# Kernel optimization log

Hardware: AMD Instinct MI355X
Metric: run time of the kernel (lower is better)

Reference implementation:

```python
import jax, jax.numpy as jnp
import numpy as np

D_MODEL = 1024
NUM_HEADS = 16
HEAD_DIM = D_MODEL // NUM_HEADS  # 64
THETA = 10000.0
B, S = 2, 2048


def setup_inputs() -> dict:
    key = jax.random.key(0)
    k1, k2, k3 = jax.random.split(key, 3)
    sigma_qkv = (2.0 / (D_MODEL + 3 * D_MODEL)) ** 0.5
    sigma_o = (2.0 / (D_MODEL + D_MODEL)) ** 0.5
    x = jax.random.normal(k1, (B, S, D_MODEL), dtype=jnp.float32)
    w_qkv = jax.random.normal(k2, (3 * D_MODEL, D_MODEL), dtype=jnp.float32) * sigma_qkv
    w_o = jax.random.normal(k3, (D_MODEL, D_MODEL), dtype=jnp.float32) * sigma_o
    token_positions = jnp.arange(S, dtype=jnp.int32)
    return {"x": x, "w_qkv": w_qkv, "w_o": w_o, "token_positions": token_positions, "mask": 1}


def _rope(t, pos):
    # t: (B, H, S, HEAD_DIM); pos: (S,) int
    ids = jnp.arange(HEAD_DIM // 2, dtype=jnp.float32)
    freqs = pos.astype(jnp.float32)[:, None] * (THETA ** (-2.0 * ids / HEAD_DIM))  # (S, HEAD_DIM/2)
    cos, sin = jnp.cos(freqs), jnp.sin(freqs)
    even, odd = t[..., 0::2], t[..., 1::2]
    r_even = even * cos - odd * sin
    r_odd = odd * cos + even * sin
    # interleave back to original layout
    return jnp.stack([r_even, r_odd], axis=-1).reshape(t.shape)


def reference(x, w_qkv, w_o, token_positions, mask):
    # fused QKV projection: Linear computes x @ W^T with W [out, in]
    qkv = x @ w_qkv.T  # (B, S, 3*D_MODEL)
    q, k, v = jnp.split(qkv, 3, axis=-1)

    def to_heads(t):
        return t.reshape(B, S, NUM_HEADS, HEAD_DIM).transpose(0, 2, 1, 3)  # (B, H, S, Dh)

    q, k, v = to_heads(q), to_heads(k), to_heads(v)
    q = _rope(q, token_positions)
    k = _rope(k, token_positions)

    scores = jnp.einsum('bhqd,bhkd->bhqk', q, k)
    if mask:  # causal: lower-triangular allowed
        causal = jnp.tril(jnp.ones((S, S), dtype=bool))
        scores = jnp.where(causal, scores, -jnp.inf)
    attn = jax.nn.softmax(scores * (HEAD_DIM ** -0.5), axis=-1)
    out = jnp.einsum('bhqk,bhkd->bhqd', attn, v)  # (B, H, S, Dh)
    out = out.transpose(0, 2, 1, 3).reshape(B, S, D_MODEL)
    return out @ w_o.T
```

## Files before the change

### kernel.cpp

```cpp
#include <hip/hip_runtime.h>
#include <hip/hip_bf16.h>
#include <math.h>

typedef __bf16 bf16_t;
typedef __bf16 bf16x8 __attribute__((ext_vector_type(8)));
typedef __bf16 bf16x4 __attribute__((ext_vector_type(4)));
typedef float  f32x4  __attribute__((ext_vector_type(4)));

#define D_MODEL 1024
#define NH      16
#define HD      64
#define BATCH   2
#define SEQ     2048
#define MROWS   (BATCH*SEQ)
#define QKVN    (3*D_MODEL)
#define FA_PAD  72
#define SCALE_LOG2E 0.18033688011112042f

__device__ __forceinline__ void async_cp16(const bf16_t* g, bf16_t* l) {
    __builtin_amdgcn_global_load_lds(
        (const __attribute__((address_space(1))) void*)g,
        (__attribute__((address_space(3))) void*)l,
        16, 0, 0);
}

__global__ void cvt_all(const float* __restrict__ x, const float* __restrict__ wq,
                        const float* __restrict__ wo,
                        bf16_t* __restrict__ xb, bf16_t* __restrict__ wqb,
                        bf16_t* __restrict__ wob) {
    const int nx = MROWS * D_MODEL, nq = QKVN * D_MODEL;
    int i = (blockIdx.x * blockDim.x + threadIdx.x) * 4;
    const float* s; bf16_t* d; int off;
    if (i < nx)           { s = x;  d = xb;  off = i; }
    else if (i < nx + nq) { s = wq; d = wqb; off = i - nx; }
    else                  { s = wo; d = wob; off = i - nx - nq; }
    float4 v = *(const float4*)(s + off);
    d[off]     = (bf16_t)v.x;
    d[off + 1] = (bf16_t)v.y;
    d[off + 2] = (bf16_t)v.z;
    d[off + 3] = (bf16_t)v.w;
}

template <typename OutT, int NI>
__global__ __launch_bounds__(256) void gemm_nt(const bf16_t* __restrict__ A,
                                               const bf16_t* __restrict__ Bm,
                                               OutT* __restrict__ C,
                                               int M, int N, int K) {
    __shared__ __align__(16) bf16_t As[128 * 32];
    __shared__ __align__(16) bf16_t Bs[NI * 32 * 32];
    const int tid  = threadIdx.x;
    const int w    = tid >> 6;
    const int lane = tid & 63;
    const int quad = lane >> 4;
    const int l16  = lane & 15;
    const int m0   = blockIdx.x * 128;
    const int n0   = blockIdx.y * (NI * 32);
    const int wm   = (w >> 1) * 64;
    const int wn   = (w & 1) * (NI * 16);

    f32x4 acc[4][NI];
    #pragma unroll
    for (int i = 0; i < 4; i++)
        #pragma unroll
        for (int j = 0; j < NI; j++)
            acc[i][j] = (f32x4){0.f, 0.f, 0.f, 0.f};

    const bf16_t* Ag0 = A  + (size_t)(m0 + (tid >> 2)) * K + (tid & 3) * 8;
    const bf16_t* Ag1 = Ag0 + (size_t)64 * K;
    const bf16_t* Bg0 = Bm + (size_t)(n0 + (tid >> 2)) * K + (tid & 3) * 8;
    const bf16_t* Bg1 = Bg0 + (size_t)64 * K;
    bf16_t* Al0 = &As[(size_t)tid * 8];
    bf16_t* Al1 = &As[((size_t)tid + 256) * 8];
    bf16_t* Bl0 = &Bs[(size_t)tid * 8];
    bf16_t* Bl1 = &Bs[((size_t)tid + 256) * 8];

    for (int k0 = 0; k0 < K; k0 += 32) {
        async_cp16(Ag0 + k0, Al0);
        async_cp16(Ag1 + k0, Al1);
        async_cp16(Bg0 + k0, Bl0);
        if (NI == 4) async_cp16(Bg1 + k0, Bl1);
        __syncthreads();

        bf16x8 af[4], bfr[NI];
        #pragma unroll
        for (int mi = 0; mi < 4; mi++)
            af[mi] = *(const bf16x8*)&As[(wm + mi * 16 + l16) * 32 + quad * 8];
        #pragma unroll
        for (int ni = 0; ni < NI; ni++)
            bfr[ni] = *(const bf16x8*)&Bs[(wn + ni * 16 + l16) * 32 + quad * 8];
        #pragma unroll
        for (int mi = 0; mi < 4; mi++)
            #pragma unroll
            for (int ni = 0; ni < NI; ni++)
                acc[mi][ni] = __builtin_amdgcn_mfma_f32_16x16x32_bf16(
                    af[mi], bfr[ni], acc[mi][ni], 0, 0, 0);
        __syncthreads();
    }

    #pragma unroll
    for (int mi = 0; mi < 4; mi++)
        #pragma unroll
        for (int ni = 0; ni < NI; ni++) {
            const int col = n0 + wn + ni * 16 + l16;
            #pragma unroll
            for (int r = 0; r < 4; r++) {
                const int row = m0 + wm + mi * 16 + quad * 4 + r;
                C[(size_t)row * N + col] = (OutT)acc[mi][ni][r];
            }
        }
}

__global__ __launch_bounds__(256) void rope_split(const bf16_t* __restrict__ qkv,
                                                  const int* __restrict__ pos,
                                                  bf16_t* __restrict__ Qh,
                                                  bf16_t* __restrict__ Kh,
                                                  bf16_t* __restrict__ VT) {
    __shared__ bf16_t vs[128][FA_PAD];
    const int tid   = threadIdx.x;
    const int s_loc = tid >> 1;
    const int half  = tid & 1;
    const int s0    = blockIdx.x * 128;
    const int bh    = blockIdx.y;
    const int b     = bh >> 4, h = bh & 15;
    const int s     = s0 + s_loc;

    const bf16_t* row = qkv + (size_t)(b * SEQ + s) * QKVN + h * HD + half * 32;

    bf16_t qbuf[32], kbuf[32], vbuf[32];
    #pragma unroll
    for (int j = 0; j < 4; j++) {
        *(bf16x8*)&qbuf[j * 8] = *(const bf16x8*)(row + j * 8);
        *(bf16x8*)&kbuf[j * 8] = *(const bf16x8*)(row + D_MODEL + j * 8);
        *(bf16x8*)&vbuf[j * 8] = *(const bf16x8*)(row + 2 * D_MODEL + j * 8);
    }

    const float pf = (float)pos[s];
    #pragma unroll
    for (int p = 0; p < 16; p++) {
        const int d2 = half * 16 + p;
        const float inv = __expf(-0.28782313662425575f * (float)d2);
        const float f = pf * inv;
        const float c = cosf(f), sn = sinf(f);
        float qe = (float)qbuf[2 * p], qo = (float)qbuf[2 * p + 1];
        float ke = (float)kbuf[2 * p], ko = (float)kbuf[2 * p + 1];
        qbuf[2 * p]     = (bf16_t)(qe * c - qo * sn);
        qbuf[2 * p + 1] = (bf16_t)(qo * c + qe * sn);
        kbuf[2 * p]     = (bf16_t)(ke * c - ko * sn);
        kbuf[2 * p + 1] = (bf16_t)(ko * c + ke * sn);
    }

    bf16_t* qdst = Qh + ((size_t)bh * SEQ + s) * HD + half * 32;
    bf16_t* kdst = Kh + ((size_t)bh * SEQ + s) * HD + half * 32;
    #pragma unroll
    for (int j = 0; j < 4; j++) {
        *(bf16x8*)(qdst + j * 8) = *(bf16x8*)&qbuf[j * 8];
        *(bf16x8*)(kdst + j * 8) = *(bf16x8*)&kbuf[j * 8];
        *(bf16x8*)&vs[s_loc][half * 32 + j * 8] = *(bf16x8*)&vbuf[j * 8];
    }
    __syncthreads();

    const int d  = tid >> 2;
    const int sc = tid & 3;
    bf16_t tmp[32];
    #pragma unroll
    for (int i = 0; i < 32; i++) tmp[i] = vs[sc * 32 + i][d];
    bf16_t* vdst = VT + ((size_t)bh * HD + d) * SEQ + s0 + sc * 32;
    #pragma unroll
    for (int j = 0; j < 4; j++)
        *(bf16x8*)(vdst + j * 8) = *(bf16x8*)&tmp[j * 8];
}

__global__ __launch_bounds__(512) void flash_attn(const bf16_t* __restrict__ Qh,
                                                  const bf16_t* __restrict__ Kh,
                                                  const bf16_t* __restrict__ VT,
                                                  bf16_t* __restrict__ AO) {
    __shared__ __align__(16) bf16_t Ks[2][64 * FA_PAD];
    __shared__ __align__(16) bf16_t Vs[2][64 * FA_PAD];
    __shared__ __align__(16) bf16_t pT[8][16][FA_PAD];

    const int tid  = threadIdx.x;
    const int w    = tid >> 6;
    const int lane = tid & 63;
    const int quad = lane >> 4;
    const int l16  = lane & 15;
    const int wq   = w & 3;
    const int g    = w >> 2;

    const int bid  = blockIdx.x;
    const int xcd  = bid & 7;
    const int mm   = bid >> 3;
    const int bh   = (mm >> 4) * 8 + xcd;
    const int pair = mm & 15;
    const int qt_big = 31 - pair;
    const int my_qt  = g ? pair : qt_big;
    const int niter  = qt_big + 1;

    const bf16_t* Qb = Qh + (size_t)bh * SEQ * HD;
    const bf16_t* Kb = Kh + (size_t)bh * SEQ * HD;
    const bf16_t* Vb = VT + (size_t)bh * HD * SEQ;

    const int q0 = my_qt * 64 + wq * 16;
    const bf16x8 aq0 = *(const bf16x8*)(Qb + (size_t)(q0 + l16) * HD + quad * 8);
    const bf16x8 aq1 = *(const bf16x8*)(Qb + (size_t)(q0 + l16) * HD + 32 + quad * 8);

    const int srow = tid >> 3, scol = (tid & 7) * 8;
    const int lds_off = srow * FA_PAD + scol;

    f32x4 o[4];
    #pragma unroll
    for (int i = 0; i < 4; i++) o[i] = (f32x4){0.f, 0.f, 0.f, 0.f};
    float lsum = 0.f;

    bf16x8 pK = *(const bf16x8*)(Kb + (size_t)srow * HD + scol);
    bf16x8 pV = *(const bf16x8*)(Vb + (size_t)srow * SEQ + scol);
    *(bf16x8*)&Ks[0][lds_off] = pK;
    *(bf16x8*)&Vs[0][lds_off] = pV;

    for (int kt = 0; kt < niter; ++kt) {
        const int cur = kt & 1;
        if (kt + 1 < niter) {
            const int kn = (kt + 1) * 64;
            pK = *(const bf16x8*)(Kb + (size_t)(kn + srow) * HD + scol);
            pV = *(const bf16x8*)(Vb + (size_t)srow * SEQ + kn + scol);
        }
        __syncthreads();

        if (kt <= my_qt) {
            const bool diag = (kt == my_qt);
            const bf16_t* KsC = &Ks[cur][0];
            const bf16_t* VsC = &Vs[cur][0];

            #pragma unroll
            for (int ni = 0; ni < 4; ni++) {
                if (diag && ni > wq) {
                    *(bf16x4*)&pT[w][l16][ni * 16 + quad * 4] = (bf16x4){0, 0, 0, 0};
                    continue;
                }
                bf16x8 kb0 = *(const bf16x8*)&KsC[(ni * 16 + l16) * FA_PAD + quad * 8];
                bf16x8 kb1 = *(const bf16x8*)&KsC[(ni * 16 + l16) * FA_PAD + 32 + quad * 8];
                f32x4 t = (f32x4){0.f, 0.f, 0.f, 0.f};
                t = __builtin_amdgcn_mfma_f32_16x16x32_bf16(kb0, aq0, t, 0, 0, 0);
                t = __builtin_amdgcn_mfma_f32_16x16x32_bf16(kb1, aq1, t, 0, 0, 0);
                bf16x4 pk;
                #pragma unroll
                for (int r = 0; r < 4; r++) {
                    float pv = exp2f(t[r] * SCALE_LOG2E);
                    if (diag && (ni * 16 + quad * 4 + r > wq * 16 + l16)) pv = 0.f;
                    lsum += pv;
                    pk[r] = (bf16_t)pv;
                }
                *(bf16x4*)&pT[w][l16][ni * 16 + quad * 4] = pk;
            }

            #pragma unroll
            for (int ks = 0; ks < 2; ks++) {
                if (diag && wq * 16 + 15 < ks * 32) continue;
                bf16x8 ap = *(const bf16x8*)&pT[w][l16][ks * 32 + quad * 8];
                #pragma unroll
                for (int ni = 0; ni < 4; ni++) {
                    bf16x8 vb = *(const bf16x8*)&VsC[(ni * 16 + l16) * FA_PAD + ks * 32 + quad * 8];
                    o[ni] = __builtin_amdgcn_mfma_f32_16x16x32_bf16(ap, vb, o[ni], 0, 0, 0);
                }
            }
        }

        if (kt + 1 < niter) {
            *(bf16x8*)&Ks[cur ^ 1][lds_off] = pK;
            *(bf16x8*)&Vs[cur ^ 1][lds_off] = pV;
        }
    }

    lsum += __shfl_xor(lsum, 16);
    lsum += __shfl_xor(lsum, 32);
    f32x4 linv;
    #pragma unroll
    for (int r = 0; r < 4; r++)
        linv[r] = 1.0f / __shfl(lsum, quad * 4 + r);

    const int b = bh >> 4, h = bh & 15;
    #pragma unroll
    for (int ni = 0; ni < 4; ni++) {
        #pragma unroll
        for (int r = 0; r < 4; r++) {
            const size_t row = (size_t)b * SEQ + q0 + quad * 4 + r;
            AO[row * D_MODEL + h * HD + ni * 16 + l16] = (bf16_t)(o[ni][r] * linv[r]);
        }
    }
}

extern "C" void kernel_launch(void* const* d_in, const int* in_sizes, int n_in,
                              void* d_out, int out_size, void* d_ws, size_t ws_size,
                              hipStream_t stream) {
    const float* x     = (const float*)d_in[0];
    const float* w_qkv = (const float*)d_in[1];
    const float* w_o   = (const float*)d_in[2];
    const int*   tpos  = (const int*)d_in[3];
    float*       out   = (float*)d_out;

    char* ws = (char*)d_ws;
    bf16_t* xb  = (bf16_t*)(ws);
    bf16_t* wqb = (bf16_t*)(ws + 8388608);
    bf16_t* wob = (bf16_t*)(ws + 14680064);
    bf16_t* qkv = (bf16_t*)(ws + 16777216);
    bf16_t* Qh  = (bf16_t*)(ws + 41943040);
    bf16_t* Kh  = (bf16_t*)(ws + 50331648);
    bf16_t* VT  = (bf16_t*)(ws + 58720256);
    bf16_t* AO  = (bf16_t*)(ws + 67108864);

    cvt_all<<<8192, 256, 0, stream>>>(x, w_qkv, w_o, xb, wqb, wob);

    gemm_nt<bf16_t, 4><<<dim3(32, 24), 256, 0, stream>>>(xb, wqb, qkv, MROWS, QKVN, D_MODEL);

    rope_split<<<dim3(SEQ / 128, BATCH * NH), 256, 0, stream>>>(qkv, tpos, Qh, Kh, VT);

    flash_attn<<<512, 512, 0, stream>>>(Qh, Kh, VT, AO);

    gemm_nt<float, 2><<<dim3(32, 16), 256, 0, stream>>>(AO, wob, out, MROWS, D_MODEL, D_MODEL);
}
```

Baseline: 201.6 us.

## Process two query row-blocks per wave in flash attention, halving block size

Each wave in the flash attention kernel now handles two 16-row query blocks instead of one, and the block shrinks from 512 to 256 threads. Each K and V fragment read from LDS is reused across two MFMA chains, which cuts LDS traffic per FLOP, and each thread loads two rows of the K/V tile. The cost is higher register pressure and fewer waves per block to hide latency, with the same grid of 512 blocks.

New measurement: 223.3 us. 10.7% more time.

```diff
diff --git a/kernel.cpp b/kernel.cpp
--- a/kernel.cpp
+++ b/kernel.cpp
@@ -170,21 +170,21 @@
         *(bf16x8*)(vdst + j * 8) = *(bf16x8*)&tmp[j * 8];
 }
 
-__global__ __launch_bounds__(512) void flash_attn(const bf16_t* __restrict__ Qh,
+__global__ __launch_bounds__(256) void flash_attn(const bf16_t* __restrict__ Qh,
                                                   const bf16_t* __restrict__ Kh,
                                                   const bf16_t* __restrict__ VT,
                                                   bf16_t* __restrict__ AO) {
     __shared__ __align__(16) bf16_t Ks[2][64 * FA_PAD];
     __shared__ __align__(16) bf16_t Vs[2][64 * FA_PAD];
-    __shared__ __align__(16) bf16_t pT[8][16][FA_PAD];
+    __shared__ __align__(16) bf16_t pT[4][2][16][FA_PAD];
 
     const int tid  = threadIdx.x;
     const int w    = tid >> 6;
     const int lane = tid & 63;
     const int quad = lane >> 4;
     const int l16  = lane & 15;
-    const int wq   = w & 3;
-    const int g    = w >> 2;
+    const int wq   = w & 1;
+    const int grp  = w >> 1;
 
     const int bid  = blockIdx.x;
     const int xcd  = bid & 7;
@@ -192,36 +192,50 @@
     const int bh   = (mm >> 4) * 8 + xcd;
     const int pair = mm & 15;
     const int qt_big = 31 - pair;
-    const int my_qt  = g ? pair : qt_big;
+    const int my_qt  = grp ? pair : qt_big;
     const int niter  = qt_big + 1;
 
     const bf16_t* Qb = Qh + (size_t)bh * SEQ * HD;
     const bf16_t* Kb = Kh + (size_t)bh * SEQ * HD;
     const bf16_t* Vb = VT + (size_t)bh * HD * SEQ;
 
-    const int q0 = my_qt * 64 + wq * 16;
-    const bf16x8 aq0 = *(const bf16x8*)(Qb + (size_t)(q0 + l16) * HD + quad * 8);
-    const bf16x8 aq1 = *(const bf16x8*)(Qb + (size_t)(q0 + l16) * HD + 32 + quad * 8);
+    const int q0t = my_qt * 64;
+    bf16x8 aq[2][2];
+    #pragma unroll
+    for (int g = 0; g < 2; g++) {
+        const int qr = q0t + (wq * 2 + g) * 16 + l16;
+        aq[g][0] = *(const bf16x8*)(Qb + (size_t)qr * HD + quad * 8);
+        aq[g][1] = *(const bf16x8*)(Qb + (size_t)qr * HD + 32 + quad * 8);
+    }
 
     const int srow = tid >> 3, scol = (tid & 7) * 8;
-    const int lds_off = srow * FA_PAD + scol;
-
-    f32x4 o[4];
-    #pragma unroll
-    for (int i = 0; i < 4; i++) o[i] = (f32x4){0.f, 0.f, 0.f, 0.f};
-    float lsum = 0.f;
-
-    bf16x8 pK = *(const bf16x8*)(Kb + (size_t)srow * HD + scol);
-    bf16x8 pV = *(const bf16x8*)(Vb + (size_t)srow * SEQ + scol);
-    *(bf16x8*)&Ks[0][lds_off] = pK;
-    *(bf16x8*)&Vs[0][lds_off] = pV;
+    const int lds_off0 = srow * FA_PAD + scol;
+    const int lds_off1 = (srow + 32) * FA_PAD + scol;
+
+    f32x4 o[2][4];
+    #pragma unroll
+    for (int g = 0; g < 2; g++)
+        #pragma unroll
+        for (int i = 0; i < 4; i++) o[g][i] = (f32x4){0.f, 0.f, 0.f, 0.f};
+    float lsum[2] = {0.f, 0.f};
+
+    bf16x8 pK0 = *(const bf16x8*)(Kb + (size_t)srow * HD + scol);
+    bf16x8 pK1 = *(const bf16x8*)(Kb + (size_t)(srow + 32) * HD + scol);
+    bf16x8 pV0 = *(const bf16x8*)(Vb + (size_t)srow * SEQ + scol);
+    bf16x8 pV1 = *(const bf16x8*)(Vb + (size_t)(srow + 32) * SEQ + scol);
+    *(bf16x8*)&Ks[0][lds_off0] = pK0;
+    *(bf16x8*)&Ks[0][lds_off1] = pK1;
+    *(bf16x8*)&Vs[0][lds_off0] = pV0;
+    *(bf16x8*)&Vs[0][lds_off1] = pV1;
 
     for (int kt = 0; kt < niter; ++kt) {
         const int cur = kt & 1;
         if (kt + 1 < niter) {
             const int kn = (kt + 1) * 64;
-            pK = *(const bf16x8*)(Kb + (size_t)(kn + srow) * HD + scol);
-            pV = *(const bf16x8*)(Vb + (size_t)srow * SEQ + kn + scol);
+            pK0 = *(const bf16x8*)(Kb + (size_t)(kn + srow) * HD + scol);
+            pK1 = *(const bf16x8*)(Kb + (size_t)(kn + srow + 32) * HD + scol);
+            pV0 = *(const bf16x8*)(Vb + (size_t)srow * SEQ + kn + scol);
+            pV1 = *(const bf16x8*)(Vb + (size_t)(srow + 32) * SEQ + kn + scol);
         }
         __syncthreads();
 
@@ -232,58 +246,80 @@
 
             #pragma unroll
             for (int ni = 0; ni < 4; ni++) {
-                if (diag && ni > wq) {
-                    *(bf16x4*)&pT[w][l16][ni * 16 + quad * 4] = (bf16x4){0, 0, 0, 0};
-                    continue;
-                }
                 bf16x8 kb0 = *(const bf16x8*)&KsC[(ni * 16 + l16) * FA_PAD + quad * 8];
                 bf16x8 kb1 = *(const bf16x8*)&KsC[(ni * 16 + l16) * FA_PAD + 32 + quad * 8];
-                f32x4 t = (f32x4){0.f, 0.f, 0.f, 0.f};
-                t = __builtin_amdgcn_mfma_f32_16x16x32_bf16(kb0, aq0, t, 0, 0, 0);
-                t = __builtin_amdgcn_mfma_f32_16x16x32_bf16(kb1, aq1, t, 0, 0, 0);
-                bf16x4 pk;
                 #pragma unroll
-                for (int r = 0; r < 4; r++) {
-                    float pv = exp2f(t[r] * SCALE_LOG2E);
-                    if (diag && (ni * 16 + quad * 4 + r > wq * 16 + l16)) pv = 0.f;
-                    lsum += pv;
-                    pk[r] = (bf16_t)pv;
+                for (int g = 0; g < 2; g++) {
+                    const int rb = wq * 2 + g;
+                    if (diag && ni > rb) {
+                        *(bf16x4*)&pT[w][g][l16][ni * 16 + quad * 4] = (bf16x4){0, 0, 0, 0};
+                        continue;
+                    }
+                    f32x4 t = (f32x4){0.f, 0.f, 0.f, 0.f};
+                    t = __builtin_amdgcn_mfma_f32_16x16x32_bf16(kb0, aq[g][0], t, 0, 0, 0);
+                    t = __builtin_amdgcn_mfma_f32_16x16x32_bf16(kb1, aq[g][1], t, 0, 0, 0);
+                    bf16x4 pk;
+                    #pragma unroll
+                    for (int r = 0; r < 4; r++) {
+                        float pv = exp2f(t[r] * SCALE_LOG2E);
+                        if (diag && (ni * 16 + quad * 4 + r > rb * 16 + l16)) pv = 0.f;
+                        lsum[g] += pv;
+                        pk[r] = (bf16_t)pv;
+                    }
+                    *(bf16x4*)&pT[w][g][l16][ni * 16 + quad * 4] = pk;
                 }
-                *(bf16x4*)&pT[w][l16][ni * 16 + quad * 4] = pk;
             }
 
             #pragma unroll
             for (int ks = 0; ks < 2; ks++) {
-                if (diag && wq * 16 + 15 < ks * 32) continue;
-                bf16x8 ap = *(const bf16x8*)&pT[w][l16][ks * 32 + quad * 8];
+                bf16x8 ap[2];
+                bool use[2];
+                #pragma unroll
+                for (int g = 0; g < 2; g++) {
+                    const int rb = wq * 2 + g;
+                    use[g] = !(diag && rb * 16 + 15 < ks * 32);
+                    if (use[g])
+                        ap[g] = *(const bf16x8*)&pT[w][g][l16][ks * 32 + quad * 8];
+                }
+                if (!use[0] && !use[1]) continue;
                 #pragma unroll
                 for (int ni = 0; ni < 4; ni++) {
                     bf16x8 vb = *(const bf16x8*)&VsC[(ni * 16 + l16) * FA_PAD + ks * 32 + quad * 8];
-                    o[ni] = __builtin_amdgcn_mfma_f32_16x16x32_bf16(ap, vb, o[ni], 0, 0, 0);
+                    #pragma unroll
+                    for (int g = 0; g < 2; g++)
+                        if (use[g])
+                            o[g][ni] = __builtin_amdgcn_mfma_f32_16x16x32_bf16(
+                                ap[g], vb, o[g][ni], 0, 0, 0);
                 }
             }
         }
 
         if (kt + 1 < niter) {
-            *(bf16x8*)&Ks[cur ^ 1][lds_off] = pK;
-            *(bf16x8*)&Vs[cur ^ 1][lds_off] = pV;
-        }
-    }
-
-    lsum += __shfl_xor(lsum, 16);
-    lsum += __shfl_xor(lsum, 32);
-    f32x4 linv;
-    #pragma unroll
-    for (int r = 0; r < 4; r++)
-        linv[r] = 1.0f / __shfl(lsum, quad * 4 + r);
+            *(bf16x8*)&Ks[cur ^ 1][lds_off0] = pK0;
+            *(bf16x8*)&Ks[cur ^ 1][lds_off1] = pK1;
+            *(bf16x8*)&Vs[cur ^ 1][lds_off0] = pV0;
+            *(bf16x8*)&Vs[cur ^ 1][lds_off1] = pV1;
+        }
+    }
 
     const int b = bh >> 4, h = bh & 15;
     #pragma unroll
-    for (int ni = 0; ni < 4; ni++) {
-        #pragma unroll
-        for (int r = 0; r < 4; r++) {
-            const size_t row = (size_t)b * SEQ + q0 + quad * 4 + r;
-            AO[row * D_MODEL + h * HD + ni * 16 + l16] = (bf16_t)(o[ni][r] * linv[r]);
+    for (int g = 0; g < 2; g++) {
+        float ls = lsum[g];
+        ls += __shfl_xor(ls, 16);
+        ls += __shfl_xor(ls, 32);
+        f32x4 linv;
+        #pragma unroll
+        for (int r = 0; r < 4; r++)
+            linv[r] = 1.0f / __shfl(ls, quad * 4 + r);
+        const int q0 = q0t + (wq * 2 + g) * 16;
+        #pragma unroll
+        for (int ni = 0; ni < 4; ni++) {
+            #pragma unroll
+            for (int r = 0; r < 4; r++) {
+                const size_t row = (size_t)b * SEQ + q0 + quad * 4 + r;
+                AO[row * D_MODEL + h * HD + ni * 16 + l16] = (bf16_t)(o[g][ni][r] * linv[r]);
+            }
         }
     }
 }
@@ -313,7 +349,7 @@
 
     rope_split<<<dim3(SEQ / 128, BATCH * NH), 256, 0, stream>>>(qkv, tpos, Qh, Kh, VT);
 
-    flash_attn<<<512, 512, 0, stream>>>(Qh, Kh, VT, AO);
+    flash_attn<<<512, 256, 0, stream>>>(Qh, Kh, VT, AO);
 
     gemm_nt<float, 2><<<dim3(32, 16), 256, 0, stream>>>(AO, wob, out, MROWS, D_MODEL, D_MODEL);
 }
```

## Deepen GEMM k-step to 64 and read K tiles directly from global in attention

Applied to the files above, without the earlier changes.

The GEMM now loads two 32-wide k-slices into separate LDS buffers per iteration, halving the number of barrier pairs and giving each wave twice as many MFMAs per sync. The flash attention kernel drops the LDS staging for K and has each wave read its K fragments straight from global memory (through cache), removing LDS writes and reads for K. This trades LDS traffic for repeated global/L2 loads of the same K tile across the eight waves, with more load latency exposed before the QK MFMAs.

Result: slower. 224.7 us (+11.4%).

```diff
diff --git a/kernel.cpp b/kernel.cpp
--- a/kernel.cpp
+++ b/kernel.cpp
@@ -46,8 +46,8 @@
                                                const bf16_t* __restrict__ Bm,
                                                OutT* __restrict__ C,
                                                int M, int N, int K) {
-    __shared__ __align__(16) bf16_t As[128 * 32];
-    __shared__ __align__(16) bf16_t Bs[NI * 32 * 32];
+    __shared__ __align__(16) bf16_t As[2][128 * 32];
+    __shared__ __align__(16) bf16_t Bs[2][NI * 32 * 32];
     const int tid  = threadIdx.x;
     const int w    = tid >> 6;
     const int lane = tid & 63;
@@ -69,31 +69,34 @@
     const bf16_t* Ag1 = Ag0 + (size_t)64 * K;
     const bf16_t* Bg0 = Bm + (size_t)(n0 + (tid >> 2)) * K + (tid & 3) * 8;
     const bf16_t* Bg1 = Bg0 + (size_t)64 * K;
-    bf16_t* Al0 = &As[(size_t)tid * 8];
-    bf16_t* Al1 = &As[((size_t)tid + 256) * 8];
-    bf16_t* Bl0 = &Bs[(size_t)tid * 8];
-    bf16_t* Bl1 = &Bs[((size_t)tid + 256) * 8];
-
-    for (int k0 = 0; k0 < K; k0 += 32) {
-        async_cp16(Ag0 + k0, Al0);
-        async_cp16(Ag1 + k0, Al1);
-        async_cp16(Bg0 + k0, Bl0);
-        if (NI == 4) async_cp16(Bg1 + k0, Bl1);
+
+    for (int k0 = 0; k0 < K; k0 += 64) {
+        #pragma unroll
+        for (int kk = 0; kk < 2; kk++) {
+            const int kc = k0 + kk * 32;
+            async_cp16(Ag0 + kc, &As[kk][(size_t)tid * 8]);
+            async_cp16(Ag1 + kc, &As[kk][((size_t)tid + 256) * 8]);
+            async_cp16(Bg0 + kc, &Bs[kk][(size_t)tid * 8]);
+            if (NI == 4) async_cp16(Bg1 + kc, &Bs[kk][((size_t)tid + 256) * 8]);
+        }
         __syncthreads();
 
-        bf16x8 af[4], bfr[NI];
-        #pragma unroll
-        for (int mi = 0; mi < 4; mi++)
-            af[mi] = *(const bf16x8*)&As[(wm + mi * 16 + l16) * 32 + quad * 8];
-        #pragma unroll
-        for (int ni = 0; ni < NI; ni++)
-            bfr[ni] = *(const bf16x8*)&Bs[(wn + ni * 16 + l16) * 32 + quad * 8];
-        #pragma unroll
-        for (int mi = 0; mi < 4; mi++)
+        #pragma unroll
+        for (int kk = 0; kk < 2; kk++) {
+            bf16x8 af[4], bfr[NI];
+            #pragma unroll
+            for (int mi = 0; mi < 4; mi++)
+                af[mi] = *(const bf16x8*)&As[kk][(wm + mi * 16 + l16) * 32 + quad * 8];
             #pragma unroll
             for (int ni = 0; ni < NI; ni++)
-                acc[mi][ni] = __builtin_amdgcn_mfma_f32_16x16x32_bf16(
-                    af[mi], bfr[ni], acc[mi][ni], 0, 0, 0);
+                bfr[ni] = *(const bf16x8*)&Bs[kk][(wn + ni * 16 + l16) * 32 + quad * 8];
+            #pragma unroll
+            for (int mi = 0; mi < 4; mi++)
+                #pragma unroll
+                for (int ni = 0; ni < NI; ni++)
+                    acc[mi][ni] = __builtin_amdgcn_mfma_f32_16x16x32_bf16(
+                        af[mi], bfr[ni], acc[mi][ni], 0, 0, 0);
+        }
         __syncthreads();
     }
 
@@ -174,7 +177,6 @@
                                                   const bf16_t* __restrict__ Kh,
                                                   const bf16_t* __restrict__ VT,
                                                   bf16_t* __restrict__ AO) {
-    __shared__ __align__(16) bf16_t Ks[2][64 * FA_PAD];
     __shared__ __align__(16) bf16_t Vs[2][64 * FA_PAD];
     __shared__ __align__(16) bf16_t pT[8][16][FA_PAD];
 
@@ -211,23 +213,20 @@
     for (int i = 0; i < 4; i++) o[i] = (f32x4){0.f, 0.f, 0.f, 0.f};
     float lsum = 0.f;
 
-    bf16x8 pK = *(const bf16x8*)(Kb + (size_t)srow * HD + scol);
     bf16x8 pV = *(const bf16x8*)(Vb + (size_t)srow * SEQ + scol);
-    *(bf16x8*)&Ks[0][lds_off] = pK;
     *(bf16x8*)&Vs[0][lds_off] = pV;
 
     for (int kt = 0; kt < niter; ++kt) {
         const int cur = kt & 1;
         if (kt + 1 < niter) {
             const int kn = (kt + 1) * 64;
-            pK = *(const bf16x8*)(Kb + (size_t)(kn + srow) * HD + scol);
             pV = *(const bf16x8*)(Vb + (size_t)srow * SEQ + kn + scol);
         }
         __syncthreads();
 
         if (kt <= my_qt) {
+            const int k0 = kt * 64;
             const bool diag = (kt == my_qt);
-            const bf16_t* KsC = &Ks[cur][0];
             const bf16_t* VsC = &Vs[cur][0];
 
             #pragma unroll
@@ -236,8 +235,9 @@
                     *(bf16x4*)&pT[w][l16][ni * 16 + quad * 4] = (bf16x4){0, 0, 0, 0};
                     continue;
                 }
-                bf16x8 kb0 = *(const bf16x8*)&KsC[(ni * 16 + l16) * FA_PAD + quad * 8];
-                bf16x8 kb1 = *(const bf16x8*)&KsC[(ni * 16 + l16) * FA_PAD + 32 + quad * 8];
+                const bf16_t* kp = Kb + (size_t)(k0 + ni * 16 + l16) * HD + quad * 8;
+                bf16x8 kb0 = *(const bf16x8*)kp;
+                bf16x8 kb1 = *(const bf16x8*)(kp + 32);
                 f32x4 t = (f32x4){0.f, 0.f, 0.f, 0.f};
                 t = __builtin_amdgcn_mfma_f32_16x16x32_bf16(kb0, aq0, t, 0, 0, 0);
                 t = __builtin_amdgcn_mfma_f32_16x16x32_bf16(kb1, aq1, t, 0, 0, 0);
@@ -264,10 +264,8 @@
             }
         }
 
-        if (kt + 1 < niter) {
-            *(bf16x8*)&Ks[cur ^ 1][lds_off] = pK;
+        if (kt + 1 < niter)
             *(bf16x8*)&Vs[cur ^ 1][lds_off] = pV;
-        }
     }
 
     lsum += __shfl_xor(lsum, 16);
```
